# Kernel optimization log

Measured on AMD Instinct MI355X. Metric: run time of the kernel, lower is better.

Reference implementation:

```python
import jax, jax.numpy as jnp
import numpy as np

N = 50000      # nodes
E = 800000     # edges (avg degree 16)
D = 64         # node feature dim
DE = 32        # edge feature dim
H = 256        # MLP hidden dim


def setup_inputs() -> dict:
    key = jax.random.key(0)
    k0, k1, k2, k3, k4 = jax.random.split(key, 5)
    x = jax.random.normal(k0, (N, D), dtype=jnp.float32)
    edge_index = jax.random.randint(k1, (2, E), 0, N)
    edge_attr = jax.random.normal(k2, (E, DE), dtype=jnp.float32)
    fan_in1 = 2 * D + DE  # 160
    W1 = jax.random.normal(k3, (fan_in1, H), dtype=jnp.float32) / np.float32(np.sqrt(fan_in1))
    b1 = jnp.zeros((H,), dtype=jnp.float32)
    W2 = jax.random.normal(k4, (H, D), dtype=jnp.float32) / np.float32(np.sqrt(H))
    b2 = jnp.zeros((D,), dtype=jnp.float32)
    return {"x": x, "edge_index": edge_index, "edge_attr": edge_attr,
            "W1": W1, "b1": b1, "W2": W2, "b2": b2}


def reference(x, edge_index, edge_attr, W1, b1, W2, b2):
    row, col = edge_index[0], edge_index[1]
    # gather endpoint features + edge features -> [E, 2D+DE]
    feats = jnp.concatenate([x[row], x[col], edge_attr], axis=-1)
    # MLP: Linear -> ReLU -> Linear
    h = jax.nn.relu(feats @ W1 + b1)          # [E, H]
    out = h @ W2 + b2                          # [E, D]
    # scatter-max aggregate by source node (row), dim_size = N
    agg = jax.ops.segment_max(out, row, num_segments=N)  # [N, D]
    # PyG's old scatter_('max') zero-fills empty slots
    agg = jnp.where(jnp.isneginf(agg), jnp.float32(0.0), agg)
    return (agg, out)
```

## Files before the change

### kernel.cpp

```cpp
#include <hip/hip_runtime.h>
#include <hip/hip_bf16.h>
#include <math.h>

#define NNODES 50000
#define NEDGES 800000
#define CHUNKS (NEDGES / 32)
#define GWAVES 4096

using short8 = __attribute__((ext_vector_type(8))) short;
using f32x4  = __attribute__((ext_vector_type(4))) float;

__device__ __forceinline__ short f2b(float v) {
    return __builtin_bit_cast(short, __float2bfloat16(v));
}

__device__ __forceinline__ unsigned pk2(short a, short b) {
    return (unsigned)(unsigned short)a | ((unsigned)(unsigned short)b << 16);
}

__global__ void prep_x(const float* __restrict__ x, short* __restrict__ xb) {
    int i = blockIdx.x * 256 + threadIdx.x;
    if (i < NNODES * 64 / 4) {
        float4 v = reinterpret_cast<const float4*>(x)[i];
        short4 o;
        o.x = f2b(v.x); o.y = f2b(v.y); o.z = f2b(v.z); o.w = f2b(v.w);
        reinterpret_cast<short4*>(xb)[i] = o;
    }
}

__global__ void prep_w(const float* __restrict__ W1, const float* __restrict__ W2,
                       short* __restrict__ wpk) {
    int i = blockIdx.x * 256 + threadIdx.x;
    if (i < 40960) {
        int k = i >> 8, n = i & 255;
        wpk[((n >> 4) * 20 + (k >> 3)) * 128 + (n & 15) * 8 + (k & 7)] = f2b(W1[i]);
    }
    if (i < 16384) {
        int k = i >> 6, n = i & 63;
        wpk[40960 + ((n >> 4) * 32 + (k >> 3)) * 128 + (n & 15) * 8 + (k & 7)] = f2b(W2[i]);
    }
}

__global__ void csr_count(const int* __restrict__ ei, unsigned* __restrict__ cnt) {
    int e = blockIdx.x * 256 + threadIdx.x;
    if (e < NEDGES) atomicAdd(&cnt[ei[e]], 1u);
}

__global__ __launch_bounds__(1024)
void csr_scan1(const unsigned* __restrict__ cnt, unsigned* __restrict__ offs,
               unsigned* __restrict__ bsum) {
    __shared__ unsigned sbuf[1024];
    int t = threadIdx.x, i = blockIdx.x * 1024 + t;
    unsigned v = (i < NNODES) ? cnt[i] : 0u;
    sbuf[t] = v;
    __syncthreads();
    for (int off = 1; off < 1024; off <<= 1) {
        unsigned add = (t >= off) ? sbuf[t - off] : 0u;
        __syncthreads();
        sbuf[t] += add;
        __syncthreads();
    }
    if (i < NNODES) offs[i] = sbuf[t];
    if (t == 1023) bsum[blockIdx.x] = sbuf[1023];
}

__global__ void csr_scan2(unsigned* __restrict__ bsum) {
    int t = threadIdx.x;
    unsigned v = (t < 49) ? bsum[t] : 0u;
    unsigned orig = v;
    for (int off = 1; off < 64; off <<= 1) {
        unsigned n = __shfl_up(v, off, 64);
        if (t >= off) v += n;
    }
    if (t < 49) bsum[t] = v - orig;
}

__global__ __launch_bounds__(1024)
void csr_scan3(const unsigned* __restrict__ cnt, unsigned* __restrict__ offs,
               const unsigned* __restrict__ bsum) {
    int i = blockIdx.x * 1024 + threadIdx.x;
    if (i < NNODES)       offs[i] = offs[i] - cnt[i] + bsum[blockIdx.x];
    else if (i == NNODES) offs[i] = NEDGES;
}

__global__ void csr_place(const int* __restrict__ ei, const unsigned* __restrict__ offs,
                          unsigned* __restrict__ cur, unsigned* __restrict__ elist) {
    int e = blockIdx.x * 256 + threadIdx.x;
    if (e < NEDGES) {
        int r = ei[e];
        unsigned p = offs[r] + atomicAdd(&cur[r], 1u);
        elist[p] = (unsigned)e;
    }
}

__global__ __launch_bounds__(1024, 4)
void edgeconv_main(const short* __restrict__ xb, const int* __restrict__ ei,
                   const float* __restrict__ ea, const short* __restrict__ wpk,
                   const float* __restrict__ b1, const float* __restrict__ b2,
                   float* __restrict__ outbuf)
{
    __shared__ short wlds[57344];
    __shared__ char  hbuf[16][2560];

    const int tid = threadIdx.x;
    for (int i = tid; i < 7168; i += 1024)
        reinterpret_cast<short8*>(wlds)[i] = reinterpret_cast<const short8*>(wpk)[i];
    __syncthreads();

    const short* w1s = wlds;
    const short* w2s = wlds + 40960;
    const int wave = tid >> 6, lane = tid & 63;
    const int l16 = lane & 15, lg = lane >> 4;
    char* hw = hbuf[wave];
    const int gw = blockIdx.x * 16 + wave;

    for (int c = gw; c < CHUNKS; c += GWAVES) {
        const int ebase = c * 32;

        short8 fx[2][5];
        #pragma unroll
        for (int nf = 0; nf < 2; ++nf) {
            int e = ebase + nf * 16 + l16;
            int r = ei[e], cc = ei[NEDGES + e];
            fx[nf][0] = *reinterpret_cast<const short8*>(xb + r * 64 + lg * 8);
            fx[nf][1] = *reinterpret_cast<const short8*>(xb + r * 64 + 32 + lg * 8);
            fx[nf][2] = *reinterpret_cast<const short8*>(xb + cc * 64 + lg * 8);
            fx[nf][3] = *reinterpret_cast<const short8*>(xb + cc * 64 + 32 + lg * 8);
            const float4* eap = reinterpret_cast<const float4*>(ea + e * 32 + lg * 8);
            float4 va = eap[0], vb = eap[1];
            short8 f;
            f[0]=f2b(va.x); f[1]=f2b(va.y); f[2]=f2b(va.z); f[3]=f2b(va.w);
            f[4]=f2b(vb.x); f[5]=f2b(vb.y); f[6]=f2b(vb.z); f[7]=f2b(vb.w);
            fx[nf][4] = f;
        }

        f32x4 acc2[4][2];
        #pragma unroll
        for (int mt2 = 0; mt2 < 4; ++mt2) {
            float4 bb = *reinterpret_cast<const float4*>(b2 + mt2 * 16 + lg * 4);
            f32x4 bi; bi[0] = bb.x; bi[1] = bb.y; bi[2] = bb.z; bi[3] = bb.w;
            acc2[mt2][0] = bi; acc2[mt2][1] = bi;
        }

        #pragma unroll 1
        for (int hp = 0; hp < 8; ++hp) {
            f32x4 acc1[2][2];
            #pragma unroll
            for (int mt = 0; mt < 2; ++mt) {
                float4 bb = *reinterpret_cast<const float4*>(b1 + hp * 32 + mt * 16 + lg * 4);
                f32x4 bi; bi[0] = bb.x; bi[1] = bb.y; bi[2] = bb.z; bi[3] = bb.w;
                acc1[mt][0] = bi; acc1[mt][1] = bi;
            }
            #pragma unroll
            for (int kk = 0; kk < 5; ++kk) {
                #pragma unroll
                for (int mt = 0; mt < 2; ++mt) {
                    int nt = hp * 2 + mt;
                    short8 wf = *reinterpret_cast<const short8*>(
                        w1s + (nt * 20 + kk * 4 + lg) * 128 + l16 * 8);
                    acc1[mt][0] = __builtin_amdgcn_mfma_f32_16x16x32_bf16(wf, fx[0][kk], acc1[mt][0], 0, 0, 0);
                    acc1[mt][1] = __builtin_amdgcn_mfma_f32_16x16x32_bf16(wf, fx[1][kk], acc1[mt][1], 0, 0, 0);
                }
            }
            #pragma unroll
            for (int mt = 0; mt < 2; ++mt) {
                #pragma unroll
                for (int nf = 0; nf < 2; ++nf) {
                    float v0 = fmaxf(acc1[mt][nf][0], 0.0f);
                    float v1 = fmaxf(acc1[mt][nf][1], 0.0f);
                    float v2 = fmaxf(acc1[mt][nf][2], 0.0f);
                    float v3 = fmaxf(acc1[mt][nf][3], 0.0f);
                    unsigned long long p =
                        (unsigned long long)pk2(f2b(v0), f2b(v1)) |
                        ((unsigned long long)pk2(f2b(v2), f2b(v3)) << 32);
                    *reinterpret_cast<unsigned long long*>(
                        hw + (nf * 16 + l16) * 80 + mt * 32 + lg * 8) = p;
                }
            }
            asm volatile("s_waitcnt lgkmcnt(0)" ::: "memory");

            short8 hfr0 = *reinterpret_cast<const short8*>(hw + l16 * 80 + lg * 16);
            short8 hfr1 = *reinterpret_cast<const short8*>(hw + (16 + l16) * 80 + lg * 16);
            #pragma unroll
            for (int mt2 = 0; mt2 < 4; ++mt2) {
                short8 wf2 = *reinterpret_cast<const short8*>(
                    w2s + (mt2 * 32 + hp * 4 + lg) * 128 + l16 * 8);
                acc2[mt2][0] = __builtin_amdgcn_mfma_f32_16x16x32_bf16(wf2, hfr0, acc2[mt2][0], 0, 0, 0);
                acc2[mt2][1] = __builtin_amdgcn_mfma_f32_16x16x32_bf16(wf2, hfr1, acc2[mt2][1], 0, 0, 0);
            }
            asm volatile("" ::: "memory");
        }

        #pragma unroll
        for (int mt2 = 0; mt2 < 4; ++mt2) {
            #pragma unroll
            for (int nf = 0; nf < 2; ++nf) {
                int e = ebase + nf * 16 + l16;
                __builtin_nontemporal_store(acc2[mt2][nf],
                    reinterpret_cast<f32x4*>(outbuf + e * 64 + mt2 * 16 + lg * 4));
            }
        }
    }
}

__global__ __launch_bounds__(256)
void agg_max(const unsigned* __restrict__ offs, const unsigned* __restrict__ elist,
             const float* __restrict__ outbuf, float* __restrict__ agg)
{
    const int wave = threadIdx.x >> 6, lane = threadIdx.x & 63;
    const int node = blockIdx.x * 4 + wave;
    if (node >= NNODES) return;
    const unsigned s = offs[node], eend = offs[node + 1];
    float m0 = -INFINITY, m1 = -INFINITY;
    unsigned p = s;
    for (; p + 2 <= eend; p += 2) {
        unsigned e0 = elist[p], e1 = elist[p + 1];
        float a = outbuf[(size_t)e0 * 64 + lane];
        float b = outbuf[(size_t)e1 * 64 + lane];
        m0 = fmaxf(m0, a);
        m1 = fmaxf(m1, b);
    }
    if (p < eend) m0 = fmaxf(m0, outbuf[(size_t)elist[p] * 64 + lane]);
    float m = fmaxf(m0, m1);
    agg[(size_t)node * 64 + lane] = (s == eend) ? 0.0f : m;
}

extern "C" void kernel_launch(void* const* d_in, const int* in_sizes, int n_in,
                              void* d_out, int out_size, void* d_ws, size_t ws_size,
                              hipStream_t stream)
{
    const float* x  = (const float*)d_in[0];
    const int*   ei = (const int*)d_in[1];
    const float* ea = (const float*)d_in[2];
    const float* W1 = (const float*)d_in[3];
    const float* b1 = (const float*)d_in[4];
    const float* W2 = (const float*)d_in[5];
    const float* b2 = (const float*)d_in[6];

    float* aggp = (float*)d_out;
    float* outp = aggp + (size_t)NNODES * 64;

    short*    xb   = (short*)d_ws;
    short*    wpk  = (short*)((char*)d_ws + 6400000);
    unsigned* meta = (unsigned*)((char*)d_ws + 6514688);
    unsigned* cnt   = meta;
    unsigned* cur   = meta + 50000;
    unsigned* offs  = meta + 100000;
    unsigned* bsum  = meta + 150016;
    unsigned* elist = meta + 150144;

    hipMemsetAsync(cnt, 0, 100000 * sizeof(unsigned), stream);
    prep_x<<<NNODES * 64 / 4 / 256, 256, 0, stream>>>(x, xb);
    prep_w<<<160, 256, 0, stream>>>(W1, W2, wpk);
    csr_count<<<NEDGES / 256, 256, 0, stream>>>(ei, cnt);
    csr_scan1<<<49, 1024, 0, stream>>>(cnt, offs, bsum);
    csr_scan2<<<1, 64, 0, stream>>>(bsum);
    csr_scan3<<<49, 1024, 0, stream>>>(cnt, offs, bsum);
    csr_place<<<NEDGES / 256, 256, 0, stream>>>(ei, offs, cur, elist);
    edgeconv_main<<<256, 1024, 0, stream>>>(xb, ei, ea, wpk, b1, b2, outp);
    agg_max<<<(NNODES + 3) / 4, 256, 0, stream>>>(offs, elist, outp, aggp);
}
```

Measured before the change: 327.2 us.

## Switch MLP to 32x32x16 MFMA with register-level hidden handoff via permlane32 swap

The edge MLP now uses 32x32x16 bf16 MFMA tiles covering all 32 edges of a chunk per instruction, with the weight packing reworked to match. The hidden activations move from the first GEMM's output layout into the second GEMM's input layout through v_permlane32_swap instead of an LDS round trip, which removes the per-wave LDS buffer and its wait. The three prep kernels are merged into one launch, the aggregation loop is unrolled to four independent max chains, and the output store is no longer nontemporal. Register pressure rises from the 16-wide accumulators, which may limit occupancy.

```diff
diff --git a/kernel.cpp b/kernel.cpp
--- a/kernel.cpp
+++ b/kernel.cpp
@@ -5,45 +5,49 @@
 #define NNODES 50000
 #define NEDGES 800000
 #define CHUNKS (NEDGES / 32)
-#define GWAVES 4096
+#define NBLK 256
+#define GWAVES (NBLK * 16)
 
 using short8 = __attribute__((ext_vector_type(8))) short;
 using f32x4  = __attribute__((ext_vector_type(4))) float;
+using f32x16 = __attribute__((ext_vector_type(16))) float;
+using u32x4  = __attribute__((ext_vector_type(4))) unsigned;
 
 __device__ __forceinline__ short f2b(float v) {
     return __builtin_bit_cast(short, __float2bfloat16(v));
 }
-
-__device__ __forceinline__ unsigned pk2(short a, short b) {
-    return (unsigned)(unsigned short)a | ((unsigned)(unsigned short)b << 16);
-}
-
-__global__ void prep_x(const float* __restrict__ x, short* __restrict__ xb) {
-    int i = blockIdx.x * 256 + threadIdx.x;
-    if (i < NNODES * 64 / 4) {
+__device__ __forceinline__ unsigned cvt2(float a, float b) {
+    return (unsigned)(unsigned short)f2b(a) | ((unsigned)(unsigned short)f2b(b) << 16);
+}
+
+__global__ void prep_all(const float* __restrict__ x, short* __restrict__ xb,
+                         const float* __restrict__ W1, const float* __restrict__ W2,
+                         short* __restrict__ wpk, const int* __restrict__ ei,
+                         unsigned* __restrict__ cnt)
+{
+    int b = blockIdx.x;
+    if (b < 3125) {
+        int i = b * 256 + threadIdx.x;
         float4 v = reinterpret_cast<const float4*>(x)[i];
         short4 o;
         o.x = f2b(v.x); o.y = f2b(v.y); o.z = f2b(v.z); o.w = f2b(v.w);
         reinterpret_cast<short4*>(xb)[i] = o;
-    }
-}
-
-__global__ void prep_w(const float* __restrict__ W1, const float* __restrict__ W2,
-                       short* __restrict__ wpk) {
-    int i = blockIdx.x * 256 + threadIdx.x;
-    if (i < 40960) {
-        int k = i >> 8, n = i & 255;
-        wpk[((n >> 4) * 20 + (k >> 3)) * 128 + (n & 15) * 8 + (k & 7)] = f2b(W1[i]);
-    }
-    if (i < 16384) {
-        int k = i >> 6, n = i & 63;
-        wpk[40960 + ((n >> 4) * 32 + (k >> 3)) * 128 + (n & 15) * 8 + (k & 7)] = f2b(W2[i]);
-    }
-}
-
-__global__ void csr_count(const int* __restrict__ ei, unsigned* __restrict__ cnt) {
-    int e = blockIdx.x * 256 + threadIdx.x;
-    if (e < NEDGES) atomicAdd(&cnt[ei[e]], 1u);
+    } else if (b < 6250) {
+        int e = (b - 3125) * 256 + threadIdx.x;
+        atomicAdd(&cnt[ei[e]], 1u);
+    } else {
+        int i = (b - 6250) * 256 + threadIdx.x;
+        if (i < 40960) {
+            int k = i >> 8, n = i & 255;
+            int lane = (n & 31) + (((k >> 3) & 1) << 5);
+            wpk[(((n >> 5) * 10 + (k >> 4)) * 64 + lane) * 8 + (k & 7)] = f2b(W1[i]);
+        }
+        if (i < 16384) {
+            int k = i >> 6, n = i & 63;
+            int lane = (n & 31) + (((k >> 3) & 1) << 5);
+            wpk[40960 + (((n >> 5) * 16 + (k >> 4)) * 64 + lane) * 8 + (k & 7)] = f2b(W2[i]);
+        }
+    }
 }
 
 __global__ __launch_bounds__(1024)
@@ -100,106 +104,94 @@
                    float* __restrict__ outbuf)
 {
     __shared__ short wlds[57344];
-    __shared__ char  hbuf[16][2560];
-
-    const int tid = threadIdx.x;
-    for (int i = tid; i < 7168; i += 1024)
+
+    for (int i = threadIdx.x; i < 7168; i += 1024)
         reinterpret_cast<short8*>(wlds)[i] = reinterpret_cast<const short8*>(wpk)[i];
     __syncthreads();
 
     const short* w1s = wlds;
     const short* w2s = wlds + 40960;
-    const int wave = tid >> 6, lane = tid & 63;
-    const int l16 = lane & 15, lg = lane >> 4;
-    char* hw = hbuf[wave];
+    const int lane = threadIdx.x & 63;
+    const int wave = threadIdx.x >> 6;
+    const int l32 = lane & 31, hi = lane >> 5;
     const int gw = blockIdx.x * 16 + wave;
 
     for (int c = gw; c < CHUNKS; c += GWAVES) {
         const int ebase = c * 32;
-
-        short8 fx[2][5];
-        #pragma unroll
-        for (int nf = 0; nf < 2; ++nf) {
-            int e = ebase + nf * 16 + l16;
-            int r = ei[e], cc = ei[NEDGES + e];
-            fx[nf][0] = *reinterpret_cast<const short8*>(xb + r * 64 + lg * 8);
-            fx[nf][1] = *reinterpret_cast<const short8*>(xb + r * 64 + 32 + lg * 8);
-            fx[nf][2] = *reinterpret_cast<const short8*>(xb + cc * 64 + lg * 8);
-            fx[nf][3] = *reinterpret_cast<const short8*>(xb + cc * 64 + 32 + lg * 8);
-            const float4* eap = reinterpret_cast<const float4*>(ea + e * 32 + lg * 8);
-            float4 va = eap[0], vb = eap[1];
-            short8 f;
-            f[0]=f2b(va.x); f[1]=f2b(va.y); f[2]=f2b(va.z); f[3]=f2b(va.w);
-            f[4]=f2b(vb.x); f[5]=f2b(vb.y); f[6]=f2b(vb.z); f[7]=f2b(vb.w);
-            fx[nf][4] = f;
-        }
-
-        f32x4 acc2[4][2];
-        #pragma unroll
-        for (int mt2 = 0; mt2 < 4; ++mt2) {
-            float4 bb = *reinterpret_cast<const float4*>(b2 + mt2 * 16 + lg * 4);
-            f32x4 bi; bi[0] = bb.x; bi[1] = bb.y; bi[2] = bb.z; bi[3] = bb.w;
-            acc2[mt2][0] = bi; acc2[mt2][1] = bi;
-        }
+        const int e = ebase + l32;
+        const int r = ei[e], cc = ei[NEDGES + e];
+
+        short8 fx[10];
+        #pragma unroll
+        for (int ks = 0; ks < 4; ++ks)
+            fx[ks] = *reinterpret_cast<const short8*>(xb + r * 64 + ks * 16 + hi * 8);
+        #pragma unroll
+        for (int ks = 0; ks < 4; ++ks)
+            fx[4 + ks] = *reinterpret_cast<const short8*>(xb + cc * 64 + ks * 16 + hi * 8);
+        #pragma unroll
+        for (int ks = 0; ks < 2; ++ks) {
+            const float4* p = reinterpret_cast<const float4*>(ea + e * 32 + ks * 16 + hi * 8);
+            float4 a = p[0], b = p[1];
+            u32x4 uu;
+            uu[0] = cvt2(a.x, a.y); uu[1] = cvt2(a.z, a.w);
+            uu[2] = cvt2(b.x, b.y); uu[3] = cvt2(b.z, b.w);
+            fx[8 + ks] = __builtin_bit_cast(short8, uu);
+        }
+
+        f32x16 acc2[2];
+        #pragma unroll
+        for (int t2 = 0; t2 < 2; ++t2)
+            #pragma unroll
+            for (int g = 0; g < 4; ++g) {
+                float4 bb = *reinterpret_cast<const float4*>(b2 + t2 * 32 + g * 8 + hi * 4);
+                acc2[t2][g * 4 + 0] = bb.x; acc2[t2][g * 4 + 1] = bb.y;
+                acc2[t2][g * 4 + 2] = bb.z; acc2[t2][g * 4 + 3] = bb.w;
+            }
 
         #pragma unroll 1
-        for (int hp = 0; hp < 8; ++hp) {
-            f32x4 acc1[2][2];
-            #pragma unroll
-            for (int mt = 0; mt < 2; ++mt) {
-                float4 bb = *reinterpret_cast<const float4*>(b1 + hp * 32 + mt * 16 + lg * 4);
-                f32x4 bi; bi[0] = bb.x; bi[1] = bb.y; bi[2] = bb.z; bi[3] = bb.w;
-                acc1[mt][0] = bi; acc1[mt][1] = bi;
-            }
-            #pragma unroll
-            for (int kk = 0; kk < 5; ++kk) {
-                #pragma unroll
-                for (int mt = 0; mt < 2; ++mt) {
-                    int nt = hp * 2 + mt;
-                    short8 wf = *reinterpret_cast<const short8*>(
-                        w1s + (nt * 20 + kk * 4 + lg) * 128 + l16 * 8);
-                    acc1[mt][0] = __builtin_amdgcn_mfma_f32_16x16x32_bf16(wf, fx[0][kk], acc1[mt][0], 0, 0, 0);
-                    acc1[mt][1] = __builtin_amdgcn_mfma_f32_16x16x32_bf16(wf, fx[1][kk], acc1[mt][1], 0, 0, 0);
-                }
-            }
-            #pragma unroll
-            for (int mt = 0; mt < 2; ++mt) {
-                #pragma unroll
-                for (int nf = 0; nf < 2; ++nf) {
-                    float v0 = fmaxf(acc1[mt][nf][0], 0.0f);
-                    float v1 = fmaxf(acc1[mt][nf][1], 0.0f);
-                    float v2 = fmaxf(acc1[mt][nf][2], 0.0f);
-                    float v3 = fmaxf(acc1[mt][nf][3], 0.0f);
-                    unsigned long long p =
-                        (unsigned long long)pk2(f2b(v0), f2b(v1)) |
-                        ((unsigned long long)pk2(f2b(v2), f2b(v3)) << 32);
-                    *reinterpret_cast<unsigned long long*>(
-                        hw + (nf * 16 + l16) * 80 + mt * 32 + lg * 8) = p;
-                }
-            }
-            asm volatile("s_waitcnt lgkmcnt(0)" ::: "memory");
-
-            short8 hfr0 = *reinterpret_cast<const short8*>(hw + l16 * 80 + lg * 16);
-            short8 hfr1 = *reinterpret_cast<const short8*>(hw + (16 + l16) * 80 + lg * 16);
-            #pragma unroll
-            for (int mt2 = 0; mt2 < 4; ++mt2) {
-                short8 wf2 = *reinterpret_cast<const short8*>(
-                    w2s + (mt2 * 32 + hp * 4 + lg) * 128 + l16 * 8);
-                acc2[mt2][0] = __builtin_amdgcn_mfma_f32_16x16x32_bf16(wf2, hfr0, acc2[mt2][0], 0, 0, 0);
-                acc2[mt2][1] = __builtin_amdgcn_mfma_f32_16x16x32_bf16(wf2, hfr1, acc2[mt2][1], 0, 0, 0);
-            }
-            asm volatile("" ::: "memory");
-        }
-
-        #pragma unroll
-        for (int mt2 = 0; mt2 < 4; ++mt2) {
-            #pragma unroll
-            for (int nf = 0; nf < 2; ++nf) {
-                int e = ebase + nf * 16 + l16;
-                __builtin_nontemporal_store(acc2[mt2][nf],
-                    reinterpret_cast<f32x4*>(outbuf + e * 64 + mt2 * 16 + lg * 4));
-            }
-        }
+        for (int t = 0; t < 8; ++t) {
+            f32x16 acc1;
+            #pragma unroll
+            for (int g = 0; g < 4; ++g) {
+                float4 bb = *reinterpret_cast<const float4*>(b1 + t * 32 + g * 8 + hi * 4);
+                acc1[g * 4 + 0] = bb.x; acc1[g * 4 + 1] = bb.y;
+                acc1[g * 4 + 2] = bb.z; acc1[g * 4 + 3] = bb.w;
+            }
+            #pragma unroll
+            for (int ks = 0; ks < 10; ++ks) {
+                short8 wf = *reinterpret_cast<const short8*>(
+                    w1s + ((t * 10 + ks) * 64 + lane) * 8);
+                acc1 = __builtin_amdgcn_mfma_f32_32x32x16_bf16(wf, fx[ks], acc1, 0, 0, 0);
+            }
+            #pragma unroll
+            for (int ksl = 0; ksl < 2; ++ksl) {
+                int q0 = ksl * 8;
+                unsigned D0 = cvt2(fmaxf(acc1[q0 + 0], 0.f), fmaxf(acc1[q0 + 1], 0.f));
+                unsigned D1 = cvt2(fmaxf(acc1[q0 + 2], 0.f), fmaxf(acc1[q0 + 3], 0.f));
+                unsigned D2 = cvt2(fmaxf(acc1[q0 + 4], 0.f), fmaxf(acc1[q0 + 5], 0.f));
+                unsigned D3 = cvt2(fmaxf(acc1[q0 + 6], 0.f), fmaxf(acc1[q0 + 7], 0.f));
+                asm volatile("v_permlane32_swap_b32 %0, %1" : "+v"(D0), "+v"(D2));
+                asm volatile("v_permlane32_swap_b32 %0, %1" : "+v"(D1), "+v"(D3));
+                u32x4 bu; bu[0] = D0; bu[1] = D1; bu[2] = D2; bu[3] = D3;
+                short8 hb = __builtin_bit_cast(short8, bu);
+
+                int ks2 = t * 2 + ksl;
+                short8 w20 = *reinterpret_cast<const short8*>(w2s + (ks2 * 64 + lane) * 8);
+                short8 w21 = *reinterpret_cast<const short8*>(w2s + ((16 + ks2) * 64 + lane) * 8);
+                acc2[0] = __builtin_amdgcn_mfma_f32_32x32x16_bf16(w20, hb, acc2[0], 0, 0, 0);
+                acc2[1] = __builtin_amdgcn_mfma_f32_32x32x16_bf16(w21, hb, acc2[1], 0, 0, 0);
+            }
+        }
+
+        #pragma unroll
+        for (int t2 = 0; t2 < 2; ++t2)
+            #pragma unroll
+            for (int g = 0; g < 4; ++g) {
+                f32x4 v;
+                v[0] = acc2[t2][g * 4 + 0]; v[1] = acc2[t2][g * 4 + 1];
+                v[2] = acc2[t2][g * 4 + 2]; v[3] = acc2[t2][g * 4 + 3];
+                *reinterpret_cast<f32x4*>(outbuf + (size_t)e * 64 + t2 * 32 + g * 8 + hi * 4) = v;
+            }
     }
 }
 
@@ -211,17 +203,18 @@
     const int node = blockIdx.x * 4 + wave;
     if (node >= NNODES) return;
     const unsigned s = offs[node], eend = offs[node + 1];
-    float m0 = -INFINITY, m1 = -INFINITY;
+    float m0 = -INFINITY, m1 = -INFINITY, m2 = -INFINITY, m3 = -INFINITY;
     unsigned p = s;
-    for (; p + 2 <= eend; p += 2) {
-        unsigned e0 = elist[p], e1 = elist[p + 1];
-        float a = outbuf[(size_t)e0 * 64 + lane];
-        float b = outbuf[(size_t)e1 * 64 + lane];
-        m0 = fmaxf(m0, a);
-        m1 = fmaxf(m1, b);
-    }
-    if (p < eend) m0 = fmaxf(m0, outbuf[(size_t)elist[p] * 64 + lane]);
-    float m = fmaxf(m0, m1);
+    for (; p + 4 <= eend; p += 4) {
+        float a = outbuf[(size_t)elist[p + 0] * 64 + lane];
+        float b = outbuf[(size_t)elist[p + 1] * 64 + lane];
+        float c = outbuf[(size_t)elist[p + 2] * 64 + lane];
+        float d = outbuf[(size_t)elist[p + 3] * 64 + lane];
+        m0 = fmaxf(m0, a); m1 = fmaxf(m1, b);
+        m2 = fmaxf(m2, c); m3 = fmaxf(m3, d);
+    }
+    for (; p < eend; ++p) m0 = fmaxf(m0, outbuf[(size_t)elist[p] * 64 + lane]);
+    float m = fmaxf(fmaxf(m0, m1), fmaxf(m2, m3));
     agg[(size_t)node * 64 + lane] = (s == eend) ? 0.0f : m;
 }
 
@@ -249,14 +242,12 @@
     unsigned* bsum  = meta + 150016;
     unsigned* elist = meta + 150144;
 
-    hipMemsetAsync(cnt, 0, 100000 * sizeof(unsigned), stream);
-    prep_x<<<NNODES * 64 / 4 / 256, 256, 0, stream>>>(x, xb);
-    prep_w<<<160, 256, 0, stream>>>(W1, W2, wpk);
-    csr_count<<<NEDGES / 256, 256, 0, stream>>>(ei, cnt);
+    (void)hipMemsetAsync(cnt, 0, 100000 * sizeof(unsigned), stream);
+    prep_all<<<6410, 256, 0, stream>>>(x, xb, W1, W2, wpk, ei, cnt);
     csr_scan1<<<49, 1024, 0, stream>>>(cnt, offs, bsum);
     csr_scan2<<<1, 64, 0, stream>>>(bsum);
     csr_scan3<<<49, 1024, 0, stream>>>(cnt, offs, bsum);
     csr_place<<<NEDGES / 256, 256, 0, stream>>>(ei, offs, cur, elist);
-    edgeconv_main<<<256, 1024, 0, stream>>>(xb, ei, ea, wpk, b1, b2, outp);
+    edgeconv_main<<<NBLK, 1024, 0, stream>>>(xb, ei, ea, wpk, b1, b2, outp);
     agg_max<<<(NNODES + 3) / 4, 256, 0, stream>>>(offs, elist, outp, aggp);
 }
```

Measured after the change: 300.8 us. -8.1%, faster.
